# Performance work log

Measured on AMD Instinct MI355X. Metric: run time of the kernel, lower is better.

The kernel has to match this reference:

```python
import jax, jax.numpy as jnp
import numpy as np

TOPK = 0.1   # effective steady-state topk (target_topk)
TAU = 0.0    # topk_tau default: pure sparse output


def setup_inputs() -> dict:
    key = jax.random.key(0)
    x = jax.random.normal(key, (64, 256, 64, 64), dtype=jnp.float32)
    return {"x": x}


def reference(x):
    # sparse_hw: keep top-k |value| positions over the H*W axis per (n, c) row.
    n, c, h, w = x.shape
    hw = h * w
    k = int(max(1, TOPK * hw))  # 409 for 64x64 at topk=0.1
    xr = x.reshape(n, c, hw)
    # torch.topk(x_reshape.abs(), k, dim=2) -> indices of k largest magnitudes
    _, idx = jax.lax.top_k(jnp.abs(xr), k)  # idx: [n, c, k]
    # mask = zeros.scatter_(2, idx, 1)
    mask = jnp.zeros_like(xr).at[
        jnp.arange(n)[:, None, None],
        jnp.arange(c)[None, :, None],
        idx,
    ].set(1.0)
    sparse_x = (mask * xr).reshape(n, c, h, w)
    if TAU == 0.0:
        return sparse_x
    # tau blend: tau * x + (1 - tau) * sparse_x
    return TAU * x + (1.0 - TAU) * sparse_x
```

## Files before the change

### kernel.cpp

```cpp
#include <hip/hip_runtime.h>

#define HW_ 4096
#define KSEL 409

__device__ __forceinline__ void scan_find(unsigned* hist, int N, unsigned kneed,
                                          unsigned* s_bin, unsigned* s_rem, int t) {
  if (t < 64) {
    const int C = N >> 6;
    const int base = N - (t + 1) * C;
    unsigned sum = 0;
    for (int j = 0; j < C; ++j) sum += hist[base + j];
    unsigned inc = sum;
    #pragma unroll
    for (int off = 1; off < 64; off <<= 1) {
      unsigned u = __shfl_up(inc, off);
      if (t >= off) inc += u;
    }
    unsigned long long m = __ballot(inc >= kneed);
    int cl = __ffsll(m) - 1;
    if (t == cl) {
      unsigned cum = inc - sum;
      for (int j = C - 1; j >= 0; --j) {
        unsigned h = hist[base + j];
        if (cum + h >= kneed) { *s_bin = (unsigned)(base + j); *s_rem = kneed - cum; break; }
        cum += h;
      }
    }
  }
}

extern "C" __global__ void __launch_bounds__(256, 4)
topk_kern(const float* __restrict__ x, float* __restrict__ out) {
  __shared__ unsigned hist[2048];
  __shared__ unsigned sb[2];
  const int t = threadIdx.x;
  const size_t rowoff = (size_t)blockIdx.x * HW_;
  const float4* xr = (const float4*)(x + rowoff);
  float4* orow = (float4*)(out + rowoff);

  float4 v[4];
  unsigned ab[16];
  #pragma unroll
  for (int j = 0; j < 4; ++j) {
    v[j] = xr[t + j * 256];
    ab[4 * j + 0] = __float_as_uint(v[j].x) & 0x7FFFFFFFu;
    ab[4 * j + 1] = __float_as_uint(v[j].y) & 0x7FFFFFFFu;
    ab[4 * j + 2] = __float_as_uint(v[j].z) & 0x7FFFFFFFu;
    ab[4 * j + 3] = __float_as_uint(v[j].w) & 0x7FFFFFFFu;
  }

  #pragma unroll
  for (int j = 0; j < 8; ++j) hist[t + j * 256] = 0;
  __syncthreads();
  #pragma unroll
  for (int i = 0; i < 16; ++i) atomicAdd(&hist[ab[i] >> 20], 1u);
  __syncthreads();
  scan_find(hist, 2048, KSEL, &sb[0], &sb[1], t);
  __syncthreads();
  const unsigned b1 = sb[0];
  const unsigned k2 = sb[1];

  #pragma unroll
  for (int j = 0; j < 4; ++j) hist[t + j * 256] = 0;
  __syncthreads();
  #pragma unroll
  for (int i = 0; i < 16; ++i)
    if ((ab[i] >> 20) == b1) atomicAdd(&hist[(ab[i] >> 10) & 0x3FFu], 1u);
  __syncthreads();
  scan_find(hist, 1024, k2, &sb[0], &sb[1], t);
  __syncthreads();
  const unsigned b2 = sb[0];
  const unsigned k3 = sb[1];
  const unsigned P = (b1 << 10) | b2;

  #pragma unroll
  for (int j = 0; j < 4; ++j) hist[t + j * 256] = 0;
  __syncthreads();
  #pragma unroll
  for (int i = 0; i < 16; ++i)
    if ((ab[i] >> 10) == P) atomicAdd(&hist[ab[i] & 0x3FFu], 1u);
  __syncthreads();
  scan_find(hist, 1024, k3, &sb[0], &sb[1], t);
  __syncthreads();
  const unsigned b3 = sb[0];
  const unsigned rem = sb[1];
  const unsigned ceq = hist[b3];
  const unsigned T = (P << 10) | b3;

  unsigned keepmask = 0;
  #pragma unroll
  for (int i = 0; i < 16; ++i) if (ab[i] > T) keepmask |= (1u << i);

  if (rem == ceq) {
    #pragma unroll
    for (int i = 0; i < 16; ++i) if (ab[i] == T) keepmask |= (1u << i);
  } else {
    __syncthreads();
    #pragma unroll
    for (int j = 0; j < 4; ++j) {
      unsigned c = 0;
      #pragma unroll
      for (int e = 0; e < 4; ++e) if (ab[4 * j + e] == T) ++c;
      hist[j * 256 + t] = c;
    }
    __syncthreads();
    if (t == 0) {
      unsigned run = 0;
      for (int i = 0; i < 1024; ++i) { unsigned h = hist[i]; hist[i] = run; run += h; }
    }
    __syncthreads();
    #pragma unroll
    for (int j = 0; j < 4; ++j) {
      unsigned r = hist[j * 256 + t];
      #pragma unroll
      for (int e = 0; e < 4; ++e) {
        if (ab[4 * j + e] == T) { if (r < rem) keepmask |= (1u << (4 * j + e)); ++r; }
      }
    }
  }

  #pragma unroll
  for (int j = 0; j < 4; ++j) {
    float4 o;
    o.x = ((keepmask >> (4 * j + 0)) & 1u) ? v[j].x : 0.0f;
    o.y = ((keepmask >> (4 * j + 1)) & 1u) ? v[j].y : 0.0f;
    o.z = ((keepmask >> (4 * j + 2)) & 1u) ? v[j].z : 0.0f;
    o.w = ((keepmask >> (4 * j + 3)) & 1u) ? v[j].w : 0.0f;
    orow[t + j * 256] = o;
  }
}

extern "C" void kernel_launch(void* const* d_in, const int* in_sizes, int n_in,
                              void* d_out, int out_size, void* d_ws, size_t ws_size,
                              hipStream_t stream) {
  const float* x = (const float*)d_in[0];
  float* out = (float*)d_out;
  const int rows = in_sizes[0] / HW_;
  topk_kern<<<dim3(rows), dim3(256), 0, stream>>>(x, out);
}
```

Before: 427.4 us.

## Use per-wave privatized histograms and a block-wide parallel scan in radix select

Replaces the single shared histogram with per-wave (or per-wave-pair) padded copies to cut LDS atomic contention. The radix split changes from 11/10/10 to 10/11/10 bits. The scan now runs across all 256 threads with vectorized uint4 LDS reads and a cross-wave combine, instead of 64 threads doing serial loops. It also raises the launch-bounds occupancy hint from 4 to 6 and recomputes absolute values on the fly instead of keeping them in registers. The trade-off is more LDS use per block and extra reduction work over the histogram copies.

```diff
diff --git a/kernel.cpp b/kernel.cpp
--- a/kernel.cpp
+++ b/kernel.cpp
@@ -2,119 +2,162 @@
 
 #define HW_ 4096
 #define KSEL 409
+#define LDSW 4128
 
-__device__ __forceinline__ void scan_find(unsigned* hist, int N, unsigned kneed,
-                                          unsigned* s_bin, unsigned* s_rem, int t) {
-  if (t < 64) {
-    const int C = N >> 6;
-    const int base = N - (t + 1) * C;
-    unsigned sum = 0;
-    for (int j = 0; j < C; ++j) sum += hist[base + j];
-    unsigned inc = sum;
+template<int NBINS, int NCOPIES, int STRIDE>
+__device__ __forceinline__ void radix_scan(const unsigned* lds, volatile unsigned* sb,
+                                           unsigned kneed, int t) {
+  constexpr int C = NBINS / 256;
+  unsigned hsum[C];
+  #pragma unroll
+  for (int j = 0; j < C; ++j) hsum[j] = 0;
+  #pragma unroll
+  for (int c = 0; c < NCOPIES; ++c) {
     #pragma unroll
-    for (int off = 1; off < 64; off <<= 1) {
-      unsigned u = __shfl_up(inc, off);
-      if (t >= off) inc += u;
-    }
-    unsigned long long m = __ballot(inc >= kneed);
-    int cl = __ffsll(m) - 1;
-    if (t == cl) {
-      unsigned cum = inc - sum;
-      for (int j = C - 1; j >= 0; --j) {
-        unsigned h = hist[base + j];
-        if (cum + h >= kneed) { *s_bin = (unsigned)(base + j); *s_rem = kneed - cum; break; }
-        cum += h;
-      }
+    for (int q = 0; q < C / 4; ++q) {
+      uint4 u = *(const uint4*)&lds[c * STRIDE + C * t + 4 * q];
+      hsum[4*q+0] += u.x; hsum[4*q+1] += u.y; hsum[4*q+2] += u.z; hsum[4*q+3] += u.w;
     }
   }
+  unsigned val = 0;
+  #pragma unroll
+  for (int j = 0; j < C; ++j) val += hsum[j];
+  const int lane = t & 63, w = t >> 6;
+  unsigned inc = val;
+  #pragma unroll
+  for (int off = 1; off < 64; off <<= 1) {
+    unsigned u = __shfl_down(inc, off);
+    if (lane + off < 64) inc += u;
+  }
+  if (lane == 0) sb[4 + w] = inc;
+  __syncthreads();
+  unsigned above_waves = 0;
+  #pragma unroll
+  for (int w2 = 0; w2 < 4; ++w2) if (w2 > w) above_waves += sb[4 + w2];
+  const unsigned P = inc + above_waves;
+  unsigned cum = P - val;
+  if (cum < kneed && kneed <= P) {
+    #pragma unroll
+    for (int j = C - 1; j >= 0; --j) {
+      unsigned h = hsum[j];
+      if (cum + h >= kneed) { sb[0] = C * t + j; sb[1] = kneed - cum; sb[2] = h; break; }
+      cum += h;
+    }
+  }
+  __syncthreads();
 }
 
-extern "C" __global__ void __launch_bounds__(256, 4)
+extern "C" __global__ void __launch_bounds__(256, 6)
 topk_kern(const float* __restrict__ x, float* __restrict__ out) {
-  __shared__ unsigned hist[2048];
-  __shared__ unsigned sb[2];
+  __shared__ unsigned lds[LDSW];
+  __shared__ unsigned sb[8];
   const int t = threadIdx.x;
+  const int w = t >> 6;
   const size_t rowoff = (size_t)blockIdx.x * HW_;
   const float4* xr = (const float4*)(x + rowoff);
   float4* orow = (float4*)(out + rowoff);
 
   float4 v[4];
-  unsigned ab[16];
   #pragma unroll
-  for (int j = 0; j < 4; ++j) {
-    v[j] = xr[t + j * 256];
-    ab[4 * j + 0] = __float_as_uint(v[j].x) & 0x7FFFFFFFu;
-    ab[4 * j + 1] = __float_as_uint(v[j].y) & 0x7FFFFFFFu;
-    ab[4 * j + 2] = __float_as_uint(v[j].z) & 0x7FFFFFFFu;
-    ab[4 * j + 3] = __float_as_uint(v[j].w) & 0x7FFFFFFFu;
-  }
+  for (int j = 0; j < 4; ++j) v[j] = xr[t + j * 256];
+  const float* pv = (const float*)v;
 
   #pragma unroll
-  for (int j = 0; j < 8; ++j) hist[t + j * 256] = 0;
+  for (int c = 0; c < 4; ++c)
+    #pragma unroll
+    for (int j = 0; j < 4; ++j) lds[c * 1032 + t + j * 256] = 0;
   __syncthreads();
-  #pragma unroll
-  for (int i = 0; i < 16; ++i) atomicAdd(&hist[ab[i] >> 20], 1u);
+  {
+    unsigned* myh = &lds[w * 1032];
+    #pragma unroll
+    for (int i = 0; i < 16; ++i) {
+      unsigned ab = __float_as_uint(pv[i]) & 0x7FFFFFFFu;
+      atomicAdd(&myh[ab >> 21], 1u);
+    }
+  }
   __syncthreads();
-  scan_find(hist, 2048, KSEL, &sb[0], &sb[1], t);
-  __syncthreads();
+  radix_scan<1024, 4, 1032>(lds, sb, KSEL, t);
   const unsigned b1 = sb[0];
   const unsigned k2 = sb[1];
 
   #pragma unroll
-  for (int j = 0; j < 4; ++j) hist[t + j * 256] = 0;
+  for (int c = 0; c < 2; ++c)
+    #pragma unroll
+    for (int j = 0; j < 8; ++j) lds[c * 2056 + t + j * 256] = 0;
   __syncthreads();
-  #pragma unroll
-  for (int i = 0; i < 16; ++i)
-    if ((ab[i] >> 20) == b1) atomicAdd(&hist[(ab[i] >> 10) & 0x3FFu], 1u);
+  {
+    unsigned* myh = &lds[(w >> 1) * 2056];
+    #pragma unroll
+    for (int i = 0; i < 16; ++i) {
+      unsigned ab = __float_as_uint(pv[i]) & 0x7FFFFFFFu;
+      if ((ab >> 21) == b1) atomicAdd(&myh[(ab >> 10) & 0x7FFu], 1u);
+    }
+  }
   __syncthreads();
-  scan_find(hist, 1024, k2, &sb[0], &sb[1], t);
-  __syncthreads();
+  radix_scan<2048, 2, 2056>(lds, sb, k2, t);
   const unsigned b2 = sb[0];
   const unsigned k3 = sb[1];
-  const unsigned P = (b1 << 10) | b2;
+  const unsigned P21 = (b1 << 11) | b2;
 
   #pragma unroll
-  for (int j = 0; j < 4; ++j) hist[t + j * 256] = 0;
+  for (int c = 0; c < 4; ++c)
+    #pragma unroll
+    for (int j = 0; j < 4; ++j) lds[c * 1032 + t + j * 256] = 0;
   __syncthreads();
-  #pragma unroll
-  for (int i = 0; i < 16; ++i)
-    if ((ab[i] >> 10) == P) atomicAdd(&hist[ab[i] & 0x3FFu], 1u);
+  {
+    unsigned* myh = &lds[w * 1032];
+    #pragma unroll
+    for (int i = 0; i < 16; ++i) {
+      unsigned ab = __float_as_uint(pv[i]) & 0x7FFFFFFFu;
+      if ((ab >> 10) == P21) atomicAdd(&myh[ab & 0x3FFu], 1u);
+    }
+  }
   __syncthreads();
-  scan_find(hist, 1024, k3, &sb[0], &sb[1], t);
-  __syncthreads();
+  radix_scan<1024, 4, 1032>(lds, sb, k3, t);
   const unsigned b3 = sb[0];
   const unsigned rem = sb[1];
-  const unsigned ceq = hist[b3];
-  const unsigned T = (P << 10) | b3;
+  const unsigned ceq = sb[2];
+  const unsigned T = (P21 << 10) | b3;
 
-  unsigned keepmask = 0;
+  unsigned keep = 0;
   #pragma unroll
-  for (int i = 0; i < 16; ++i) if (ab[i] > T) keepmask |= (1u << i);
+  for (int i = 0; i < 16; ++i) {
+    unsigned ab = __float_as_uint(pv[i]) & 0x7FFFFFFFu;
+    if (ab > T) keep |= (1u << i);
+  }
 
   if (rem == ceq) {
     #pragma unroll
-    for (int i = 0; i < 16; ++i) if (ab[i] == T) keepmask |= (1u << i);
+    for (int i = 0; i < 16; ++i) {
+      unsigned ab = __float_as_uint(pv[i]) & 0x7FFFFFFFu;
+      if (ab == T) keep |= (1u << i);
+    }
   } else {
     __syncthreads();
+    unsigned* eqh = (unsigned*)lds;
     #pragma unroll
     for (int j = 0; j < 4; ++j) {
       unsigned c = 0;
       #pragma unroll
-      for (int e = 0; e < 4; ++e) if (ab[4 * j + e] == T) ++c;
-      hist[j * 256 + t] = c;
+      for (int e = 0; e < 4; ++e)
+        if ((__float_as_uint(pv[4*j+e]) & 0x7FFFFFFFu) == T) ++c;
+      eqh[j * 256 + t] = c;
     }
     __syncthreads();
     if (t == 0) {
       unsigned run = 0;
-      for (int i = 0; i < 1024; ++i) { unsigned h = hist[i]; hist[i] = run; run += h; }
+      for (int i = 0; i < 1024; ++i) { unsigned h = eqh[i]; eqh[i] = run; run += h; }
     }
     __syncthreads();
     #pragma unroll
     for (int j = 0; j < 4; ++j) {
-      unsigned r = hist[j * 256 + t];
+      unsigned r = eqh[j * 256 + t];
       #pragma unroll
       for (int e = 0; e < 4; ++e) {
-        if (ab[4 * j + e] == T) { if (r < rem) keepmask |= (1u << (4 * j + e)); ++r; }
+        if ((__float_as_uint(pv[4*j+e]) & 0x7FFFFFFFu) == T) {
+          if (r < rem) keep |= (1u << (4*j + e));
+          ++r;
+        }
       }
     }
   }
@@ -122,10 +165,10 @@
   #pragma unroll
   for (int j = 0; j < 4; ++j) {
     float4 o;
-    o.x = ((keepmask >> (4 * j + 0)) & 1u) ? v[j].x : 0.0f;
-    o.y = ((keepmask >> (4 * j + 1)) & 1u) ? v[j].y : 0.0f;
-    o.z = ((keepmask >> (4 * j + 2)) & 1u) ? v[j].z : 0.0f;
-    o.w = ((keepmask >> (4 * j + 3)) & 1u) ? v[j].w : 0.0f;
+    o.x = ((keep >> (4*j+0)) & 1u) ? v[j].x : 0.0f;
+    o.y = ((keep >> (4*j+1)) & 1u) ? v[j].y : 0.0f;
+    o.z = ((keep >> (4*j+2)) & 1u) ? v[j].z : 0.0f;
+    o.w = ((keep >> (4*j+3)) & 1u) ? v[j].w : 0.0f;
     orow[t + j * 256] = o;
   }
 }
```

New measurement: 432.4 us. Within noise of the previous version (+1.2%).
